# Kernel tuning notes

Hardware: AMD Instinct MI355X
Metric: run time of the kernel (lower is better)

The kernel has to match this reference:

```python
import jax, jax.numpy as jnp
import numpy as np

N_CELL, N_TISSUE, H, NH = 200000, 2000, 256, 8
HD = H // NH
SCALE = HD ** -0.5
EPS = 1e-5


def _layernorm(x, g, b):
    m = jnp.mean(x, axis=-1, keepdims=True)
    v = jnp.mean((x - m) ** 2, axis=-1, keepdims=True)
    return (x - m) / jnp.sqrt(v + EPS) * g + b


def setup_inputs() -> dict:
    key = jax.random.key(0)
    ks = jax.random.split(key, 12)
    s = 0.02

    def lin(k):
        k1, k2 = jax.random.split(k)
        return (jax.random.normal(k1, (H, H), jnp.float32) * s,
                jax.random.normal(k2, (H,), jnp.float32) * s)

    Wq_bu, bq_bu = lin(ks[0])
    Wk_bu, bk_bu = lin(ks[1])
    Wv_bu, bv_bu = lin(ks[2])
    Wo_bu, bo_bu = lin(ks[3])
    Wv_td, bv_td = lin(ks[4])
    Wo_td, bo_td = lin(ks[5])
    return dict(
        cell_features=jax.random.normal(ks[6], (N_CELL, H), jnp.float32),
        tissue_features=jax.random.normal(ks[7], (N_TISSUE, H), jnp.float32),
        cluster_labels=jax.random.randint(ks[8], (N_CELL,), 0, N_TISSUE, dtype=jnp.int32),
        tissue_batch=jnp.zeros((N_TISSUE,), jnp.int32),
        Wq_bu=Wq_bu, bq_bu=bq_bu, Wk_bu=Wk_bu, bk_bu=bk_bu,
        Wv_bu=Wv_bu, bv_bu=bv_bu, Wo_bu=Wo_bu, bo_bu=bo_bu,
        Wv_td=Wv_td, bv_td=bv_td, Wo_td=Wo_td, bo_td=bo_td,
        ln_cell_g=jnp.ones((H,), jnp.float32), ln_cell_b=jnp.zeros((H,), jnp.float32),
        ln_tissue_g=jnp.ones((H,), jnp.float32), ln_tissue_b=jnp.zeros((H,), jnp.float32),
    )


def reference(cell_features, tissue_features, cluster_labels, tissue_batch,
              Wq_bu, bq_bu, Wk_bu, bk_bu, Wv_bu, bv_bu, Wo_bu, bo_bu,
              Wv_td, bv_td, Wo_td, bo_td,
              ln_cell_g, ln_cell_b, ln_tissue_g, ln_tissue_b):
    Nc = cell_features.shape[0]
    Nt = tissue_features.shape[0]

    # ---- bottom-up: each tissue node (1 query) attends over its cells (segment attention) ----
    Q = (tissue_features @ Wq_bu + bq_bu).reshape(Nt, NH, HD)   # [Nt, h, d]
    K = (cell_features @ Wk_bu + bk_bu).reshape(Nc, NH, HD)     # [Nc, h, d]
    V = (cell_features @ Wv_bu + bv_bu).reshape(Nc, NH, HD)     # [Nc, h, d]

    # per-cell score against its own cluster's tissue query
    scores = jnp.einsum('nhd,nhd->nh', K, Q[cluster_labels]) * SCALE  # [Nc, h]
    smax = jax.lax.stop_gradient(
        jax.ops.segment_max(scores, cluster_labels, num_segments=Nt))  # [Nt, h]
    ex = jnp.exp(scores - smax[cluster_labels])
    denom = jax.ops.segment_sum(ex, cluster_labels, num_segments=Nt)   # [Nt, h]
    w = ex / denom[cluster_labels]                                     # [Nc, h]
    attended = jax.ops.segment_sum(w[..., None] * V, cluster_labels,
                                   num_segments=Nt)                    # [Nt, h, d]
    attended = attended.reshape(Nt, H) @ Wo_bu + bo_bu

    counts = jax.ops.segment_sum(jnp.ones((Nc,), cell_features.dtype),
                                 cluster_labels, num_segments=Nt)
    tissue_updated = jnp.where(counts[:, None] > 0, attended, tissue_features)

    # ---- top-down: each cell attends to its single tissue token ----
    # softmax over a single key is identically 1, so q/k projections cancel:
    # attended_cell = out_proj(v_proj(tissue_updated[cluster]))
    td_per_tissue = (tissue_updated @ Wv_td + bv_td) @ Wo_td + bo_td   # [Nt, H]
    cell_updated = td_per_tissue[cluster_labels]                       # [Nc, H]

    cell_out = _layernorm(cell_features + cell_updated, ln_cell_g, ln_cell_b)
    tissue_out = _layernorm(tissue_features + tissue_updated, ln_tissue_g, ln_tissue_b)
    return (cell_out, tissue_out)
```

## Files before the change

kernel.cpp:

```cpp
#include <hip/hip_runtime.h>
#include <math.h>

#define NC 200000
#define NT 2000
#define HH 256
#define NH_ 8
#define SCALE 0.17677669529663687f
#define EPS 1e-5f
#define SLICE 128
#define PSLICES (NT + NC / SLICE + 1)
#define PSTRIDE 2056


__global__ void k_hist(const int* __restrict__ labels, int* __restrict__ counts) {
  int i = blockIdx.x * 256 + threadIdx.x;
  if (i < NC) atomicAdd(&counts[labels[i]], 1);
}

__global__ void k_scan(const int* __restrict__ counts, int* __restrict__ offsets,
                       int* __restrict__ soff, int* __restrict__ slice_t) {
  int tid = threadIdx.x;
  int base = tid * 32;
  int la[32], lb[32], scnt[32];
  int sa = 0, sb = 0;
  #pragma unroll
  for (int k = 0; k < 32; k++) {
    int idx = base + k;
    int v = (idx < NT) ? counts[idx] : 0;
    la[k] = sa; lb[k] = sb;
    scnt[k] = (v + SLICE - 1) / SLICE;
    sa += v; sb += scnt[k];
  }
  int ia_ = sa, ib_ = sb;
  #pragma unroll
  for (int d = 1; d < 64; d <<= 1) {
    int oa = __shfl_up(ia_, d, 64);
    int ob = __shfl_up(ib_, d, 64);
    if (tid >= d) { ia_ += oa; ib_ += ob; }
  }
  int ea = ia_ - sa, eb = ib_ - sb;
  #pragma unroll
  for (int k = 0; k < 32; k++) {
    int idx = base + k;
    if (idx < NT) {
      offsets[idx] = ea + la[k];
      soff[idx] = eb + lb[k];
      int st = eb + lb[k];
      for (int s2 = 0; s2 < scnt[k]; s2++) slice_t[st + s2] = idx;
    }
  }
  if (tid == 63) { offsets[NT] = ia_; soff[NT] = ib_; }
}

__global__ void k_scatter(const int* __restrict__ labels, const int* __restrict__ offsets,
                          int* __restrict__ cursor, int* __restrict__ cindex) {
  int i = blockIdx.x * 256 + threadIdx.x;
  if (i < NC) {
    int c = labels[i];
    int pos = offsets[c] + atomicAdd(&cursor[c], 1);
    cindex[pos] = i;
  }
}


__global__ __launch_bounds__(256) void k_gemm_bias(
    const float* __restrict__ A, const float* __restrict__ W,
    const float* __restrict__ bias, float* __restrict__ C, int M)
{
  __shared__ float Al[16][33];
  __shared__ float Wl[32][HH];
  int tid = threadIdx.x;
  int r0 = blockIdx.x * 16;
  float acc[16];
  #pragma unroll
  for (int r = 0; r < 16; r++) acc[r] = 0.f;
  for (int k0 = 0; k0 < HH; k0 += 32) {
    for (int e = tid; e < 16 * 32; e += 256) {
      int r = e >> 5, k = e & 31;
      int row = r0 + r;
      Al[r][k] = (row < M) ? A[(size_t)row * HH + k0 + k] : 0.f;
    }
    for (int e = tid; e < 32 * HH; e += 256) {
      int k = e >> 8, j = e & 255;
      Wl[k][j] = W[(size_t)(k0 + k) * HH + j];
    }
    __syncthreads();
    for (int k = 0; k < 32; k++) {
      float w = Wl[k][tid];
      #pragma unroll
      for (int r = 0; r < 16; r++) acc[r] += Al[r][k] * w;
    }
    __syncthreads();
  }
  float bj = bias[tid];
  #pragma unroll
  for (int r = 0; r < 16; r++) {
    int row = r0 + r;
    if (row < M) C[(size_t)row * HH + tid] = acc[r] + bj;
  }
}


__global__ __launch_bounds__(256) void k_qproj(
    const float* __restrict__ Q, const float* __restrict__ Wk,
    const float* __restrict__ bk, float* __restrict__ Qproj,
    float* __restrict__ bkq)
{
  __shared__ float Al[64][33];
  __shared__ float Bl[32][257];
  int h = blockIdx.x & 7, tb = blockIdx.x >> 3;
  int t0 = tb * 64;
  int tid = threadIdx.x;
  for (int e = tid; e < 64 * 32; e += 256) {
    int r = e >> 5, d = e & 31;
    int t = t0 + r;
    Al[r][d] = (t < NT) ? Q[(size_t)t * HH + h * 32 + d] * SCALE : 0.f;
  }
  for (int e = tid; e < 256 * 32; e += 256) {
    int j = e >> 5, d = e & 31;
    Bl[d][j] = Wk[(size_t)j * HH + h * 32 + d];
  }
  __syncthreads();
  float acc[64];
  #pragma unroll
  for (int r = 0; r < 64; r++) acc[r] = 0.f;
  for (int d = 0; d < 32; d++) {
    float b = Bl[d][tid];
    #pragma unroll
    for (int r = 0; r < 64; r++) acc[r] += Al[r][d] * b;
  }
  for (int r = 0; r < 64; r++) {
    int t = t0 + r;
    if (t < NT) Qproj[((size_t)t * NH_ + h) * HH + tid] = acc[r];
  }
  if (tid < 64) {
    int t = t0 + tid;
    if (t < NT) {
      float s = 0.f;
      #pragma unroll
      for (int d = 0; d < 32; d++) s += Al[tid][d] * bk[h * 32 + d];
      bkq[t * NH_ + h] = s;
    }
  }
}


__global__ __launch_bounds__(256) void k_cellslice(
    const float* __restrict__ cell, const int* __restrict__ cindex,
    const int* __restrict__ offsets, const int* __restrict__ soff,
    const int* __restrict__ slice_t,
    const float* __restrict__ Qproj, const float* __restrict__ bkq,
    float* __restrict__ Pbuf)
{
  __shared__ int   cidx[SLICE];
  __shared__ float cwlds[NH_][HH];
  __shared__ float red[4][NH_];

  int s = blockIdx.x;
  if (s >= soff[NT]) return;
  int t = slice_t[s];
  int l = s - soff[t];
  int c0 = offsets[t] + l * SLICE;
  int c1 = min(c0 + SLICE, offsets[t + 1]);
  int nc = c1 - c0;
  int ncp = (nc + 3) & ~3;

  int tid = threadIdx.x;
  int w = tid >> 6, lane = tid & 63;
  int hg = lane & 3, kc = lane >> 2;

  if (tid < SLICE) cidx[tid] = cindex[min(c0 + tid, c1 - 1)];

  const float* qpb = Qproj + (size_t)t * NH_ * HH;
  float4 qp0[4], qp1[4];
  #pragma unroll
  for (int i = 0; i < 4; i++) {
    qp0[i] = *reinterpret_cast<const float4*>(qpb + (2 * hg) * HH + (i * 16 + kc) * 4);
    qp1[i] = *reinterpret_cast<const float4*>(qpb + (2 * hg + 1) * HH + (i * 16 + kc) * 4);
  }
  float bq0 = bkq[t * NH_ + 2 * hg];
  float bq1 = bkq[t * NH_ + 2 * hg + 1];

  float4 cw0[4], cw1[4];
  #pragma unroll
  for (int i = 0; i < 4; i++) {
    cw0[i] = make_float4(0.f, 0.f, 0.f, 0.f);
    cw1[i] = make_float4(0.f, 0.f, 0.f, 0.f);
  }
  float d0 = 0.f, d1 = 0.f;

  __syncthreads();

  float4 x[4], xn[4];
  {
    const float* r = cell + (size_t)cidx[min(w, nc - 1)] * HH;
    #pragma unroll
    for (int i = 0; i < 4; i++)
      x[i] = *reinterpret_cast<const float4*>(r + (i * 16 + kc) * 4);
  }

  for (int ic = w; ic < ncp; ic += 4) {
    int icn = min(ic + 4, nc - 1);
    const float* rn = cell + (size_t)cidx[icn] * HH;
    #pragma unroll
    for (int i = 0; i < 4; i++)
      xn[i] = *reinterpret_cast<const float4*>(rn + (i * 16 + kc) * 4);

    float s0 = 0.f, s1 = 0.f;
    #pragma unroll
    for (int i = 0; i < 4; i++) {
      s0 += x[i].x * qp0[i].x + x[i].y * qp0[i].y + x[i].z * qp0[i].z + x[i].w * qp0[i].w;
      s1 += x[i].x * qp1[i].x + x[i].y * qp1[i].y + x[i].z * qp1[i].z + x[i].w * qp1[i].w;
    }
    #pragma unroll
    for (int d = 4; d < 64; d <<= 1) {
      s0 += __shfl_xor(s0, d, 64);
      s1 += __shfl_xor(s1, d, 64);
    }
    float e0 = __expf(s0 + bq0);
    float e1 = __expf(s1 + bq1);
    if (ic >= nc) { e0 = 0.f; e1 = 0.f; }
    d0 += e0; d1 += e1;
    #pragma unroll
    for (int i = 0; i < 4; i++) {
      cw0[i].x += e0 * x[i].x; cw0[i].y += e0 * x[i].y;
      cw0[i].z += e0 * x[i].z; cw0[i].w += e0 * x[i].w;
      cw1[i].x += e1 * x[i].x; cw1[i].y += e1 * x[i].y;
      cw1[i].z += e1 * x[i].z; cw1[i].w += e1 * x[i].w;
    }
    #pragma unroll
    for (int i = 0; i < 4; i++) x[i] = xn[i];
  }

  if (w == 0) {
    #pragma unroll
    for (int i = 0; i < 4; i++) {
      *reinterpret_cast<float4*>(&cwlds[2 * hg][(i * 16 + kc) * 4]) = cw0[i];
      *reinterpret_cast<float4*>(&cwlds[2 * hg + 1][(i * 16 + kc) * 4]) = cw1[i];
    }
  }
  if (kc == 0) { red[w][2 * hg] = d0; red[w][2 * hg + 1] = d1; }
  __syncthreads();
  #pragma unroll
  for (int ww = 1; ww < 4; ww++) {
    if (w == ww) {
      #pragma unroll
      for (int i = 0; i < 4; i++) {
        float4 a = *reinterpret_cast<float4*>(&cwlds[2 * hg][(i * 16 + kc) * 4]);
        a.x += cw0[i].x; a.y += cw0[i].y; a.z += cw0[i].z; a.w += cw0[i].w;
        *reinterpret_cast<float4*>(&cwlds[2 * hg][(i * 16 + kc) * 4]) = a;
        float4 b = *reinterpret_cast<float4*>(&cwlds[2 * hg + 1][(i * 16 + kc) * 4]);
        b.x += cw1[i].x; b.y += cw1[i].y; b.z += cw1[i].z; b.w += cw1[i].w;
        *reinterpret_cast<float4*>(&cwlds[2 * hg + 1][(i * 16 + kc) * 4]) = b;
      }
    }
    __syncthreads();
  }

  float* pb = Pbuf + (size_t)s * PSTRIDE;
  #pragma unroll
  for (int h = 0; h < NH_; h++) pb[h * HH + tid] = cwlds[h][tid];
  if (tid < NH_) pb[2048 + tid] = red[0][tid] + red[1][tid] + red[2][tid] + red[3][tid];
}


#define TCH 4

__global__ __launch_bounds__(256) void k_tissuechain(
    const float* __restrict__ tissue, const int* __restrict__ counts,
    const float* __restrict__ Pbuf, const int* __restrict__ soff,
    const float* __restrict__ Wv, const float* __restrict__ bv,
    const float* __restrict__ Wo, const float* __restrict__ bo,
    const float* __restrict__ Wvtd, const float* __restrict__ bvtd,
    const float* __restrict__ Wotd, const float* __restrict__ botd,
    const float* __restrict__ lng, const float* __restrict__ lnb,
    float* __restrict__ td, float* __restrict__ out_tissue)
{
  __shared__ float s_cwn[TCH][NH_ * HH];
  __shared__ float s_a[TCH][HH];
  __shared__ float s_tu[TCH][HH];
  __shared__ float s_tmp[TCH][HH];
  __shared__ float s_red[2][4];
  __shared__ float s_dinv[TCH][NH_];
  int t0 = blockIdx.x * TCH;
  int j = threadIdx.x;
  int h = j >> 5;

  if (j < TCH * NH_) {
    int t = j >> 3, hh = j & 7;
    int s0 = soff[t0 + t], s1 = soff[t0 + t + 1];
    float d = 0.f;
    for (int q = s0; q < s1; q++) d += Pbuf[(size_t)q * PSTRIDE + 2048 + hh];
    s_dinv[t][hh] = (s1 > s0) ? 1.f / d : 0.f;
  }
  __syncthreads();

  for (int e = j; e < TCH * NH_ * HH; e += 256) {
    int t = e >> 11, c = e & 2047, hh = c >> 8;
    int s0 = soff[t0 + t], s1 = soff[t0 + t + 1];
    float a = 0.f;
    for (int q = s0; q < s1; q++) a += Pbuf[(size_t)q * PSTRIDE + c];
    s_cwn[t][c] = a * s_dinv[t][hh];
  }
  __syncthreads();

  float acc[TCH];
  #pragma unroll
  for (int t = 0; t < TCH; t++) acc[t] = 0.f;
  for (int k = 0; k < HH; k++) {
    float w = Wv[(size_t)k * HH + j];
    #pragma unroll
    for (int t = 0; t < TCH; t++) acc[t] += s_cwn[t][h * HH + k] * w;
  }
  {
    float bj = bv[j];
    #pragma unroll
    for (int t = 0; t < TCH; t++) s_a[t][j] = acc[t] + bj;
  }
  __syncthreads();

  #pragma unroll
  for (int t = 0; t < TCH; t++) acc[t] = 0.f;
  for (int k = 0; k < HH; k++) {
    float w = Wo[(size_t)k * HH + j];
    #pragma unroll
    for (int t = 0; t < TCH; t++) acc[t] += s_a[t][k] * w;
  }
  {
    float bj = bo[j];
    #pragma unroll
    for (int t = 0; t < TCH; t++) {
      int tt = t0 + t;
      s_tu[t][j] = (counts[tt] > 0) ? (acc[t] + bj) : tissue[(size_t)tt * HH + j];
    }
  }
  __syncthreads();

  #pragma unroll
  for (int t = 0; t < TCH; t++) acc[t] = 0.f;
  for (int k = 0; k < HH; k++) {
    float w = Wvtd[(size_t)k * HH + j];
    #pragma unroll
    for (int t = 0; t < TCH; t++) acc[t] += s_tu[t][k] * w;
  }
  {
    float bj = bvtd[j];
    #pragma unroll
    for (int t = 0; t < TCH; t++) s_tmp[t][j] = acc[t] + bj;
  }
  __syncthreads();

  #pragma unroll
  for (int t = 0; t < TCH; t++) acc[t] = 0.f;
  for (int k = 0; k < HH; k++) {
    float w = Wotd[(size_t)k * HH + j];
    #pragma unroll
    for (int t = 0; t < TCH; t++) acc[t] += s_tmp[t][k] * w;
  }
  {
    float bj = botd[j];
    #pragma unroll
    for (int t = 0; t < TCH; t++) td[(size_t)(t0 + t) * HH + j] = acc[t] + bj;
  }

  float gj = lng[j], bj2 = lnb[j];
  for (int t = 0; t < TCH; t++) {
    float y = tissue[(size_t)(t0 + t) * HH + j] + s_tu[t][j];
    float s1 = y, s2 = y * y;
    #pragma unroll
    for (int d = 1; d < 64; d <<= 1) { s1 += __shfl_xor(s1, d, 64); s2 += __shfl_xor(s2, d, 64); }
    int wv_ = j >> 6, ln_ = j & 63;
    __syncthreads();
    if (ln_ == 0) { s_red[0][wv_] = s1; s_red[1][wv_] = s2; }
    __syncthreads();
    s1 = s_red[0][0] + s_red[0][1] + s_red[0][2] + s_red[0][3];
    s2 = s_red[1][0] + s_red[1][1] + s_red[1][2] + s_red[1][3];
    float mean = s1 * (1.f / 256.f);
    float var = s2 * (1.f / 256.f) - mean * mean;
    float inv = rsqrtf(var + EPS);
    out_tissue[(size_t)(t0 + t) * HH + j] = (y - mean) * inv * gj + bj2;
  }
}


#define COB 2048

__global__ __launch_bounds__(256) void k_cellout(
    const float* __restrict__ cell, const float* __restrict__ td,
    const int* __restrict__ labels,
    const float* __restrict__ lng, const float* __restrict__ lnb,
    float* __restrict__ out)
{
  int lane = threadIdx.x & 63;
  float4 gv = *reinterpret_cast<const float4*>(&lng[lane * 4]);
  float4 bv = *reinterpret_cast<const float4*>(&lnb[lane * 4]);
  int wid = blockIdx.x * 4 + (threadIdx.x >> 6);
  for (int row = wid; row < NC; row += COB * 4) {
    int c = labels[row];
    float4 x = *reinterpret_cast<const float4*>(&cell[(size_t)row * HH + lane * 4]);
    float4 u = *reinterpret_cast<const float4*>(&td[(size_t)c * HH + lane * 4]);
    float y0 = x.x + u.x, y1 = x.y + u.y, y2 = x.z + u.z, y3 = x.w + u.w;
    float s1 = y0 + y1 + y2 + y3;
    float s2 = y0 * y0 + y1 * y1 + y2 * y2 + y3 * y3;
    #pragma unroll
    for (int d = 1; d < 64; d <<= 1) { s1 += __shfl_xor(s1, d, 64); s2 += __shfl_xor(s2, d, 64); }
    float mean = s1 * (1.f / 256.f);
    float var = s2 * (1.f / 256.f) - mean * mean;
    float inv = rsqrtf(var + EPS);
    float4 o;
    o.x = (y0 - mean) * inv * gv.x + bv.x;
    o.y = (y1 - mean) * inv * gv.y + bv.y;
    o.z = (y2 - mean) * inv * gv.z + bv.z;
    o.w = (y3 - mean) * inv * gv.w + bv.w;
    *reinterpret_cast<float4*>(&out[(size_t)row * HH + lane * 4]) = o;
  }
}


extern "C" void kernel_launch(void* const* d_in, const int* in_sizes, int n_in,
                              void* d_out, int out_size, void* d_ws, size_t ws_size,
                              hipStream_t stream) {
  const float* cell   = (const float*)d_in[0];
  const float* tissue = (const float*)d_in[1];
  const int*   labels = (const int*)d_in[2];
  const float* Wq = (const float*)d_in[4];  const float* bq = (const float*)d_in[5];
  const float* Wk = (const float*)d_in[6];  const float* bk = (const float*)d_in[7];
  const float* Wv = (const float*)d_in[8];  const float* bv = (const float*)d_in[9];
  const float* Wo = (const float*)d_in[10]; const float* bo = (const float*)d_in[11];
  const float* Wvtd = (const float*)d_in[12]; const float* bvtd = (const float*)d_in[13];
  const float* Wotd = (const float*)d_in[14]; const float* botd = (const float*)d_in[15];
  const float* lncg = (const float*)d_in[16]; const float* lncb = (const float*)d_in[17];
  const float* lntg = (const float*)d_in[18]; const float* lntb = (const float*)d_in[19];
  float* out_cell   = (float*)d_out;
  float* out_tissue = (float*)d_out + (size_t)NC * HH;

  char* w = (char*)d_ws;
  auto take = [&](size_t bytes) { void* p = (void*)w; w += (bytes + 255) & ~(size_t)255; return p; };
  int*   counts  = (int*)take((size_t)NT * 4);
  int*   cursor  = (int*)take((size_t)NT * 4);
  int*   offsets = (int*)take((size_t)(NT + 1) * 4);
  int*   soff    = (int*)take((size_t)(NT + 1) * 4);
  int*   slice_t = (int*)take((size_t)PSLICES * 4);
  int*   cindex  = (int*)take((size_t)NC * 4);
  float* Q       = (float*)take((size_t)NT * HH * 4);
  float* Qproj   = (float*)take((size_t)NT * NH_ * HH * 4);
  float* bkq     = (float*)take((size_t)NT * NH_ * 4);
  float* td      = (float*)take((size_t)NT * HH * 4);
  float* Pbuf    = (float*)take((size_t)PSLICES * PSTRIDE * 4);

  hipMemsetAsync(counts, 0, 16384, stream);

  const int CB = (NC + 255) / 256;
  k_hist<<<CB, 256, 0, stream>>>(labels, counts);
  k_scan<<<1, 64, 0, stream>>>(counts, offsets, soff, slice_t);
  k_scatter<<<CB, 256, 0, stream>>>(labels, offsets, cursor, cindex);

  k_gemm_bias<<<(NT + 15) / 16, 256, 0, stream>>>(tissue, Wq, bq, Q, NT);
  k_qproj<<<8 * ((NT + 63) / 64), 256, 0, stream>>>(Q, Wk, bk, Qproj, bkq);

  k_cellslice<<<PSLICES, 256, 0, stream>>>(cell, cindex, offsets, soff, slice_t,
                                           Qproj, bkq, Pbuf);

  k_tissuechain<<<NT / TCH, 256, 0, stream>>>(tissue, counts, Pbuf, soff,
      Wv, bv, Wo, bo, Wvtd, bvtd, Wotd, botd, lntg, lntb, td, out_tissue);

  k_cellout<<<COB, 256, 0, stream>>>(cell, td, labels, lncg, lncb, out_cell);
}
```

Measured before the change: 405.0 us.

## Stage gathered cell rows through LDS with coalesced loads; dual-row cellout

The segment-attention kernel now has each wave gather groups of four cell rows with fully coalesced float4 loads (one row per wave instruction), stage them in a padded per-wave LDS buffer, and prefetch the next group into registers while computing on the current one. This replaces the earlier per-lane strided gather, which needed many 16-byte loads per row, and aims to raise memory-level parallelism. The cell-output LayerNorm kernel doubles its grid and processes two rows per iteration so more loads are in flight. The cost is extra LDS traffic and about 16KB more shared memory per block, which may lower occupancy.

```diff
diff --git a/kernel.cpp b/kernel.cpp
--- a/kernel.cpp
+++ b/kernel.cpp
@@ -145,6 +145,9 @@
 }
 
 
+#define GRP 4
+#define ROWF 260
+
 __global__ __launch_bounds__(256) void k_cellslice(
     const float* __restrict__ cell, const int* __restrict__ cindex,
     const int* __restrict__ offsets, const int* __restrict__ soff,
@@ -153,6 +156,7 @@
     float* __restrict__ Pbuf)
 {
   __shared__ int   cidx[SLICE];
+  __shared__ float xbuf[4][GRP][ROWF];
   __shared__ float cwlds[NH_][HH];
   __shared__ float red[4][NH_];
 
@@ -163,7 +167,6 @@
   int c0 = offsets[t] + l * SLICE;
   int c1 = min(c0 + SLICE, offsets[t + 1]);
   int nc = c1 - c0;
-  int ncp = (nc + 3) & ~3;
 
   int tid = threadIdx.x;
   int w = tid >> 6, lane = tid & 63;
@@ -191,45 +194,64 @@
 
   __syncthreads();
 
-  float4 x[4], xn[4];
-  {
-    const float* r = cell + (size_t)cidx[min(w, nc - 1)] * HH;
-    #pragma unroll
-    for (int i = 0; i < 4; i++)
-      x[i] = *reinterpret_cast<const float4*>(r + (i * 16 + kc) * 4);
-  }
-
-  for (int ic = w; ic < ncp; ic += 4) {
-    int icn = min(ic + 4, nc - 1);
-    const float* rn = cell + (size_t)cidx[icn] * HH;
-    #pragma unroll
-    for (int i = 0; i < 4; i++)
-      xn[i] = *reinterpret_cast<const float4*>(rn + (i * 16 + kc) * 4);
-
-    float s0 = 0.f, s1 = 0.f;
-    #pragma unroll
-    for (int i = 0; i < 4; i++) {
-      s0 += x[i].x * qp0[i].x + x[i].y * qp0[i].y + x[i].z * qp0[i].z + x[i].w * qp0[i].w;
-      s1 += x[i].x * qp1[i].x + x[i].y * qp1[i].y + x[i].z * qp1[i].z + x[i].w * qp1[i].w;
-    }
-    #pragma unroll
-    for (int d = 4; d < 64; d <<= 1) {
-      s0 += __shfl_xor(s0, d, 64);
-      s1 += __shfl_xor(s1, d, 64);
-    }
-    float e0 = __expf(s0 + bq0);
-    float e1 = __expf(s1 + bq1);
-    if (ic >= nc) { e0 = 0.f; e1 = 0.f; }
-    d0 += e0; d1 += e1;
-    #pragma unroll
-    for (int i = 0; i < 4; i++) {
-      cw0[i].x += e0 * x[i].x; cw0[i].y += e0 * x[i].y;
-      cw0[i].z += e0 * x[i].z; cw0[i].w += e0 * x[i].w;
-      cw1[i].x += e1 * x[i].x; cw1[i].y += e1 * x[i].y;
-      cw1[i].z += e1 * x[i].z; cw1[i].w += e1 * x[i].w;
-    }
-    #pragma unroll
-    for (int i = 0; i < 4; i++) x[i] = xn[i];
+  float (*myx)[ROWF] = xbuf[w];
+  int base = w * GRP;
+  float4 st[GRP];
+
+  #pragma unroll
+  for (int r = 0; r < GRP; r++)
+    st[r] = *reinterpret_cast<const float4*>(
+        &cell[(size_t)cidx[min(base + r, nc - 1)] * HH + lane * 4]);
+  #pragma unroll
+  for (int r = 0; r < GRP; r++)
+    *reinterpret_cast<float4*>(&myx[r][lane * 4]) = st[r];
+
+  for (int gb = base; gb < nc; gb += 16) {
+    int gn = gb + 16;
+    bool more = gn < nc;
+    if (more) {
+      #pragma unroll
+      for (int r = 0; r < GRP; r++)
+        st[r] = *reinterpret_cast<const float4*>(
+            &cell[(size_t)cidx[min(gn + r, nc - 1)] * HH + lane * 4]);
+    }
+    #pragma unroll
+    for (int c = 0; c < GRP; c++) {
+      float4 x0 = *reinterpret_cast<float4*>(&myx[c][(0 * 16 + kc) * 4]);
+      float4 x1 = *reinterpret_cast<float4*>(&myx[c][(1 * 16 + kc) * 4]);
+      float4 x2 = *reinterpret_cast<float4*>(&myx[c][(2 * 16 + kc) * 4]);
+      float4 x3 = *reinterpret_cast<float4*>(&myx[c][(3 * 16 + kc) * 4]);
+      float s0 = x0.x * qp0[0].x + x0.y * qp0[0].y + x0.z * qp0[0].z + x0.w * qp0[0].w
+               + x1.x * qp0[1].x + x1.y * qp0[1].y + x1.z * qp0[1].z + x1.w * qp0[1].w
+               + x2.x * qp0[2].x + x2.y * qp0[2].y + x2.z * qp0[2].z + x2.w * qp0[2].w
+               + x3.x * qp0[3].x + x3.y * qp0[3].y + x3.z * qp0[3].z + x3.w * qp0[3].w;
+      float s1 = x0.x * qp1[0].x + x0.y * qp1[0].y + x0.z * qp1[0].z + x0.w * qp1[0].w
+               + x1.x * qp1[1].x + x1.y * qp1[1].y + x1.z * qp1[1].z + x1.w * qp1[1].w
+               + x2.x * qp1[2].x + x2.y * qp1[2].y + x2.z * qp1[2].z + x2.w * qp1[2].w
+               + x3.x * qp1[3].x + x3.y * qp1[3].y + x3.z * qp1[3].z + x3.w * qp1[3].w;
+      #pragma unroll
+      for (int d = 4; d < 64; d <<= 1) {
+        s0 += __shfl_xor(s0, d, 64);
+        s1 += __shfl_xor(s1, d, 64);
+      }
+      float e0 = __expf(s0 + bq0);
+      float e1 = __expf(s1 + bq1);
+      if (gb + c >= nc) { e0 = 0.f; e1 = 0.f; }
+      d0 += e0; d1 += e1;
+      cw0[0].x += e0 * x0.x; cw0[0].y += e0 * x0.y; cw0[0].z += e0 * x0.z; cw0[0].w += e0 * x0.w;
+      cw0[1].x += e0 * x1.x; cw0[1].y += e0 * x1.y; cw0[1].z += e0 * x1.z; cw0[1].w += e0 * x1.w;
+      cw0[2].x += e0 * x2.x; cw0[2].y += e0 * x2.y; cw0[2].z += e0 * x2.z; cw0[2].w += e0 * x2.w;
+      cw0[3].x += e0 * x3.x; cw0[3].y += e0 * x3.y; cw0[3].z += e0 * x3.z; cw0[3].w += e0 * x3.w;
+      cw1[0].x += e1 * x0.x; cw1[0].y += e1 * x0.y; cw1[0].z += e1 * x0.z; cw1[0].w += e1 * x0.w;
+      cw1[1].x += e1 * x1.x; cw1[1].y += e1 * x1.y; cw1[1].z += e1 * x1.z; cw1[1].w += e1 * x1.w;
+      cw1[2].x += e1 * x2.x; cw1[2].y += e1 * x2.y; cw1[2].z += e1 * x2.z; cw1[2].w += e1 * x2.w;
+      cw1[3].x += e1 * x3.x; cw1[3].y += e1 * x3.y; cw1[3].z += e1 * x3.z; cw1[3].w += e1 * x3.w;
+    }
+    if (more) {
+      #pragma unroll
+      for (int r = 0; r < GRP; r++)
+        *reinterpret_cast<float4*>(&myx[r][lane * 4]) = st[r];
+    }
   }
 
   if (w == 0) {
@@ -383,7 +405,7 @@
 }
 
 
-#define COB 2048
+#define COB 4096
 
 __global__ __launch_bounds__(256) void k_cellout(
     const float* __restrict__ cell, const float* __restrict__ td,
@@ -393,26 +415,53 @@
 {
   int lane = threadIdx.x & 63;
   float4 gv = *reinterpret_cast<const float4*>(&lng[lane * 4]);
-  float4 bv = *reinterpret_cast<const float4*>(&lnb[lane * 4]);
+  float4 bvv = *reinterpret_cast<const float4*>(&lnb[lane * 4]);
+  const int stride = COB * 4;
   int wid = blockIdx.x * 4 + (threadIdx.x >> 6);
-  for (int row = wid; row < NC; row += COB * 4) {
-    int c = labels[row];
-    float4 x = *reinterpret_cast<const float4*>(&cell[(size_t)row * HH + lane * 4]);
-    float4 u = *reinterpret_cast<const float4*>(&td[(size_t)c * HH + lane * 4]);
-    float y0 = x.x + u.x, y1 = x.y + u.y, y2 = x.z + u.z, y3 = x.w + u.w;
-    float s1 = y0 + y1 + y2 + y3;
-    float s2 = y0 * y0 + y1 * y1 + y2 * y2 + y3 * y3;
-    #pragma unroll
-    for (int d = 1; d < 64; d <<= 1) { s1 += __shfl_xor(s1, d, 64); s2 += __shfl_xor(s2, d, 64); }
-    float mean = s1 * (1.f / 256.f);
-    float var = s2 * (1.f / 256.f) - mean * mean;
-    float inv = rsqrtf(var + EPS);
-    float4 o;
-    o.x = (y0 - mean) * inv * gv.x + bv.x;
-    o.y = (y1 - mean) * inv * gv.y + bv.y;
-    o.z = (y2 - mean) * inv * gv.z + bv.z;
-    o.w = (y3 - mean) * inv * gv.w + bv.w;
-    *reinterpret_cast<float4*>(&out[(size_t)row * HH + lane * 4]) = o;
+  for (int row = wid; row < NC; row += 2 * stride) {
+    int rowB = row + stride;
+    bool hasB = rowB < NC;
+    int cA = labels[row];
+    float4 xA = *reinterpret_cast<const float4*>(&cell[(size_t)row * HH + lane * 4]);
+    float4 uA = *reinterpret_cast<const float4*>(&td[(size_t)cA * HH + lane * 4]);
+    float4 xB, uB;
+    if (hasB) {
+      int cB = labels[rowB];
+      xB = *reinterpret_cast<const float4*>(&cell[(size_t)rowB * HH + lane * 4]);
+      uB = *reinterpret_cast<const float4*>(&td[(size_t)cB * HH + lane * 4]);
+    }
+    {
+      float y0 = xA.x + uA.x, y1 = xA.y + uA.y, y2 = xA.z + uA.z, y3 = xA.w + uA.w;
+      float s1 = y0 + y1 + y2 + y3;
+      float s2 = y0 * y0 + y1 * y1 + y2 * y2 + y3 * y3;
+      #pragma unroll
+      for (int d = 1; d < 64; d <<= 1) { s1 += __shfl_xor(s1, d, 64); s2 += __shfl_xor(s2, d, 64); }
+      float mean = s1 * (1.f / 256.f);
+      float var = s2 * (1.f / 256.f) - mean * mean;
+      float inv = rsqrtf(var + EPS);
+      float4 o;
+      o.x = (y0 - mean) * inv * gv.x + bvv.x;
+      o.y = (y1 - mean) * inv * gv.y + bvv.y;
+      o.z = (y2 - mean) * inv * gv.z + bvv.z;
+      o.w = (y3 - mean) * inv * gv.w + bvv.w;
+      *reinterpret_cast<float4*>(&out[(size_t)row * HH + lane * 4]) = o;
+    }
+    if (hasB) {
+      float y0 = xB.x + uB.x, y1 = xB.y + uB.y, y2 = xB.z + uB.z, y3 = xB.w + uB.w;
+      float s1 = y0 + y1 + y2 + y3;
+      float s2 = y0 * y0 + y1 * y1 + y2 * y2 + y3 * y3;
+      #pragma unroll
+      for (int d = 1; d < 64; d <<= 1) { s1 += __shfl_xor(s1, d, 64); s2 += __shfl_xor(s2, d, 64); }
+      float mean = s1 * (1.f / 256.f);
+      float var = s2 * (1.f / 256.f) - mean * mean;
+      float inv = rsqrtf(var + EPS);
+      float4 o;
+      o.x = (y0 - mean) * inv * gv.x + bvv.x;
+      o.y = (y1 - mean) * inv * gv.y + bvv.y;
+      o.z = (y2 - mean) * inv * gv.z + bvv.z;
+      o.w = (y3 - mean) * inv * gv.w + bvv.w;
+      *reinterpret_cast<float4*>(&out[(size_t)rowB * HH + lane * 4]) = o;
+    }
   }
 }
 
```

Result: slower. 441.8 us (+9.1%).
